# Performance work log

Hardware: AMD Instinct MI355X
Metric: run time of the kernel (lower is better)

## Reference

```python
import jax, jax.numpy as jnp
import numpy as np

B, T, C = 4, 2048, 1024
H, D = 16, 64  # num_heads, head_size; H*D == C


def setup_inputs() -> dict:
    key = jax.random.key(0)
    k1, k2, k3 = jax.random.split(key, 3)
    x = jax.random.normal(k1, (B, T, C), dtype=jnp.float32)
    w_qkv = jax.random.normal(k2, (C, 3 * C), dtype=jnp.float32) * (C ** -0.5)
    w_out = jax.random.normal(k3, (C, C), dtype=jnp.float32) * (C ** -0.5)
    b_out = jnp.zeros((C,), dtype=jnp.float32)
    return {"x": x, "w_qkv": w_qkv, "w_out": w_out, "b_out": b_out}


def reference(x, w_qkv, w_out, b_out):
    Bb, Tt, Cc = x.shape
    qkv = x @ w_qkv                        # [B,T,3C]
    q, k, v = jnp.split(qkv, 3, axis=2)
    # [B,T,C] -> [B,H,T,D]
    q = q.reshape(Bb, Tt, H, D).transpose(0, 2, 1, 3)
    k = k.reshape(Bb, Tt, H, D).transpose(0, 2, 1, 3)
    v = v.reshape(Bb, Tt, H, D).transpose(0, 2, 1, 3)
    scores = jnp.einsum('bhqd,bhkd->bhqk', q, k) * (D ** -0.5)
    causal = jnp.tril(jnp.ones((Tt, Tt), dtype=bool))
    scores = jnp.where(causal, scores, -jnp.inf)
    attn = jax.nn.softmax(scores, axis=-1)  # dropout is identity in eval mode
    out = jnp.einsum('bhqk,bhkd->bhqd', attn, v)
    out = out.transpose(0, 2, 1, 3).reshape(Bb, Tt, Cc)
    return out @ w_out + b_out
```

## Files before the change

### kernel.cpp

```cpp
#include <hip/hip_runtime.h>

typedef __bf16 bf16;
typedef __bf16 bf16x4 __attribute__((ext_vector_type(4)));
typedef __bf16 bf16x8 __attribute__((ext_vector_type(8)));
typedef float  f32x4  __attribute__((ext_vector_type(4)));

#define MFMA16(A_, B_, C_) __builtin_amdgcn_mfma_f32_16x16x32_bf16((A_), (B_), (C_), 0, 0, 0)

#define BB 4
#define TT 2048
#define CC 1024
#define HH 16
#define DD 64
#define MM (BB * TT)
#define N_QKV (3 * CC)
#define LDSS 72
#define BSTRIDE 36
#define QSCALE2 0.18033688f

#define BARRIER() do { asm volatile("" ::: "memory"); \
                       __builtin_amdgcn_s_barrier();  \
                       asm volatile("" ::: "memory"); } while (0)
#define VMCNT(n)  asm volatile("s_waitcnt vmcnt(" #n ")" ::: "memory")

static __device__ __forceinline__ void store_lds8(bf16* p, bf16x8 v) {
  bf16x4 lo, hi;
#pragma unroll
  for (int i = 0; i < 4; i++) { lo[i] = v[i]; hi[i] = v[i + 4]; }
  *(bf16x4*)p = lo;
  *(bf16x4*)(p + 4) = hi;
}

static __device__ __forceinline__ bf16x8 load_lds8(const bf16* p) {
  bf16x4 lo = *(const bf16x4*)p;
  bf16x4 hi = *(const bf16x4*)(p + 4);
  bf16x8 v;
#pragma unroll
  for (int i = 0; i < 4; i++) { v[i] = lo[i]; v[i + 4] = hi[i]; }
  return v;
}

static __device__ __forceinline__ void async_cp16(const bf16* g, bf16* l) {
  __builtin_amdgcn_global_load_lds(
      (const __attribute__((address_space(1))) void*)g,
      (__attribute__((address_space(3))) void*)l, 16, 0, 0);
}

__global__ __launch_bounds__(256) void sniff_k(const unsigned short* __restrict__ u,
                                               int* __restrict__ flag) {
  __shared__ int s;
  if (threadIdx.x == 0) s = 0;
  __syncthreads();
  int c = 0;
  for (int i = threadIdx.x; i < 65536; i += 256)
    if ((u[i] & 0x7F80u) == 0x7F80u) c = 1;
  if (c) atomicOr(&s, 1);
  __syncthreads();
  if (threadIdx.x == 0) *flag = s;
}

__global__ __launch_bounds__(256) void cvt_k(const void* __restrict__ in,
                                             bf16* __restrict__ out,
                                             const int* __restrict__ flag,
                                             size_t off) {
  const int fl = *flag;
  const size_t i = ((size_t)blockIdx.x * 256 + threadIdx.x) * 8;
  if (fl) {
    f32x4 a = *(const f32x4*)((const float*)in + off + i);
    f32x4 b = *(const f32x4*)((const float*)in + off + i + 4);
    bf16x8 o;
#pragma unroll
    for (int j = 0; j < 4; j++) { o[j] = (bf16)a[j]; o[4 + j] = (bf16)b[j]; }
    *(bf16x8*)(out + i) = o;
  } else {
    *(bf16x8*)(out + i) = *(const bf16x8*)((const bf16*)in + off + i);
  }
}

__global__ __launch_bounds__(256) void transpose_k(const void* __restrict__ in,
                                                   bf16* __restrict__ out,
                                                   int R, int C,
                                                   const int* __restrict__ flag) {
  __shared__ bf16 tile[32][33];
  const int fl = *flag;
  const int c0 = blockIdx.x * 32, r0 = blockIdx.y * 32;
  const int tx = threadIdx.x & 31, ty = threadIdx.x >> 5;
#pragma unroll
  for (int i = ty; i < 32; i += 8) {
    const size_t idx = (size_t)(r0 + i) * C + c0 + tx;
    tile[i][tx] = fl ? (bf16)((const float*)in)[idx] : ((const bf16*)in)[idx];
  }
  __syncthreads();
#pragma unroll
  for (int i = ty; i < 32; i += 8)
    out[(size_t)(c0 + i) * R + r0 + tx] = tile[tx][i];
}

__global__ __launch_bounds__(256) void vtrans_k(const bf16* __restrict__ qkv,
                                                bf16* __restrict__ vt) {
  __shared__ bf16 tile[32][33];
  const int bh = blockIdx.z;
  const int t0 = blockIdx.x * 32, d0 = blockIdx.y * 32;
  const bf16* src = qkv + (size_t)(bh >> 4) * TT * N_QKV + 2 * CC + (bh & 15) * DD;
  const int tx = threadIdx.x & 31, ty = threadIdx.x >> 5;
#pragma unroll
  for (int i = ty; i < 32; i += 8)
    tile[i][tx] = src[(size_t)(t0 + i) * N_QKV + d0 + tx];
  __syncthreads();
  bf16* dst = vt + ((size_t)bh * DD + d0) * TT + t0;
#pragma unroll
  for (int i = ty; i < 32; i += 8)
    dst[(size_t)i * TT + tx] = tile[tx][i];
}

template <int EPI>
__global__ __launch_bounds__(512, 2) void gemm8p(const bf16* __restrict__ A,
                                                 const bf16* __restrict__ Bt,
                                                 const void* __restrict__ biasv,
                                                 void* __restrict__ Cv,
                                                 const int* __restrict__ flag,
                                                 int M, int N, int K,
                                                 int lda, int ldc) {
  __shared__ __align__(16) bf16 sA[2][256 * 64];
  __shared__ __align__(16) bf16 sB[2][256 * 64];
  const int fl = *flag;
  const int tid = threadIdx.x;
  const int lane = tid & 63, wave = tid >> 6;
  const int quad = lane >> 4, l15 = lane & 15;
  const int wm = wave >> 2, wn = wave & 3;

  const int nm = M >> 8;
  const int cpx = gridDim.x >> 3;
  const int sw = ((int)blockIdx.x & 7) * cpx + ((int)blockIdx.x >> 3);
  const int m0 = (sw % nm) * 256, n0 = (sw / nm) * 256;

  const int s_row = wave * 8 + (lane >> 3);
  const int s_col = ((((lane & 7) * 16) ^ ((lane >> 3) << 4)) >> 1);

  f32x4 acc[8][4];
#pragma unroll
  for (int i = 0; i < 8; i++)
#pragma unroll
    for (int j = 0; j < 4; j++) {
      f32x4 z = {0.f, 0.f, 0.f, 0.f};
      acc[i][j] = z;
    }

  const bf16* Asrc = A + (size_t)(m0 + s_row) * lda + s_col;
  const bf16* Bsrc = Bt + (size_t)(n0 + s_row) * K + s_col;

#define STAGE8(buf_, k0_)                                                  \
  do {                                                                     \
    _Pragma("unroll")                                                      \
    for (int i_ = 0; i_ < 4; i_++)                                         \
      async_cp16(Asrc + (size_t)(i_ * 64) * lda + (k0_),                   \
                 &sA[buf_][i_ * 4096 + wave * 512]);                       \
    _Pragma("unroll")                                                      \
    for (int i_ = 0; i_ < 4; i_++)                                         \
      async_cp16(Bsrc + (size_t)(i_ * 64) * K + (k0_),                     \
                 &sB[buf_][i_ * 4096 + wave * 512]);                       \
  } while (0)

  const int swz = (l15 & 7) << 3;

#define COMPUTE8(buf_)                                                       \
  do {                                                                       \
    _Pragma("unroll")                                                        \
    for (int kk = 0; kk < 2; kk++) {                                         \
      bf16x8 bfr[4];                                                         \
      _Pragma("unroll")                                                      \
      for (int nf = 0; nf < 4; nf++) {                                       \
        const int rB = wn * 64 + nf * 16 + l15;                              \
        bfr[nf] = *(const bf16x8*)(&sB[buf_][rB * 64 +                       \
                                             ((kk * 32 + quad * 8) ^ swz)]); \
      }                                                                      \
      _Pragma("unroll")                                                      \
      for (int mh = 0; mh < 2; mh++) {                                       \
        bf16x8 af[4];                                                        \
        _Pragma("unroll")                                                    \
        for (int mf = 0; mf < 4; mf++) {                                     \
          const int rA = wm * 128 + (mh * 4 + mf) * 16 + l15;                \
          af[mf] = *(const bf16x8*)(&sA[buf_][rA * 64 +                      \
                                              ((kk * 32 + quad * 8) ^ swz)]);\
        }                                                                    \
        _Pragma("unroll")                                                    \
        for (int mf = 0; mf < 4; mf++)                                       \
          _Pragma("unroll")                                                  \
          for (int nf = 0; nf < 4; nf++)                                     \
            acc[mh * 4 + mf][nf] =                                           \
                MFMA16(af[mf], bfr[nf], acc[mh * 4 + mf][nf]);               \
      }                                                                      \
    }                                                                        \
  } while (0)

  const int NT = K >> 6;
  STAGE8(0, 0);
  STAGE8(1, 64);
  VMCNT(8);
  BARRIER();

  for (int t = 0; t < NT; t += 2) {
    COMPUTE8(0);
    BARRIER();
    if (t + 2 < NT) { STAGE8(0, (t + 2) * 64); VMCNT(8); }
    else            { VMCNT(0); }
    BARRIER();
    COMPUTE8(1);
    BARRIER();
    if (t + 3 < NT) { STAGE8(1, (t + 3) * 64); VMCNT(8); }
    else            { VMCNT(0); }
    BARRIER();
  }

#undef STAGE8
#undef COMPUTE8

#pragma unroll
  for (int mf = 0; mf < 8; mf++) {
#pragma unroll
    for (int r = 0; r < 4; r++) {
      const int m = m0 + wm * 128 + mf * 16 + quad * 4 + r;
#pragma unroll
      for (int nf = 0; nf < 4; nf++) {
        const int n = n0 + wn * 64 + nf * 16 + l15;
        float v = acc[mf][nf][r];
        const size_t idx = (size_t)m * ldc + n;
        if (EPI == 1) {
          v += fl ? ((const float*)biasv)[n] : (float)((const bf16*)biasv)[n];
          if (fl) ((float*)Cv)[idx] = v;
          else    ((bf16*)Cv)[idx] = (bf16)v;
        } else {
          ((bf16*)Cv)[idx] = (bf16)v;
        }
      }
    }
  }
}

template <int EPI>
__global__ __launch_bounds__(256) void gemm_lds(const bf16* __restrict__ A,
                                                const bf16* __restrict__ Bt,
                                                const void* __restrict__ biasv,
                                                void* __restrict__ Cv,
                                                const int* __restrict__ flag,
                                                size_t aoff, size_t coff,
                                                int M, int N, int K,
                                                int lda, int ldc) {
  const int fl = *flag;
  __shared__ __align__(16) bf16 sA[128 * 32];
  __shared__ __align__(16) bf16 sB[128 * 32];
  const int tid = threadIdx.x;
  const int lane = tid & 63, wave = tid >> 6;
  const int quad = lane >> 4, l15 = lane & 15;
  const int wr = wave >> 1, wc = wave & 1;
  const int m0 = blockIdx.x * 128, n0 = blockIdx.y * 128;
  const int grow = lane >> 2;
  const int gcol = (lane & 3) * 8;

  f32x4 acc[4][4];
#pragma unroll
  for (int i = 0; i < 4; i++)
#pragma unroll
    for (int j = 0; j < 4; j++) {
      f32x4 z = {0.f, 0.f, 0.f, 0.f};
      acc[i][j] = z;
    }

  const bf16* Ag = A + aoff + (size_t)(m0 + wave * 32 + grow) * lda + gcol;
  const bf16* Bg = Bt + (size_t)(n0 + wave * 32 + grow) * K + gcol;
  bf16* sAw = sA + wave * 32 * 32;
  bf16* sBw = sB + wave * 32 * 32;

  for (int k0 = 0; k0 < K; k0 += 32) {
    __syncthreads();
    async_cp16(Ag, sAw);
    async_cp16(Ag + (size_t)16 * lda, sAw + 16 * 32);
    async_cp16(Bg, sBw);
    async_cp16(Bg + (size_t)16 * K, sBw + 16 * 32);
    Ag += 32;
    Bg += 32;
    __syncthreads();

    bf16x8 af[4], bfr[4];
#pragma unroll
    for (int mi = 0; mi < 4; mi++)
      af[mi] = *(const bf16x8*)(sA + (wr * 64 + mi * 16 + l15) * 32 + quad * 8);
#pragma unroll
    for (int ni = 0; ni < 4; ni++)
      bfr[ni] = *(const bf16x8*)(sB + (wc * 64 + ni * 16 + l15) * 32 + quad * 8);
#pragma unroll
    for (int mi = 0; mi < 4; mi++)
#pragma unroll
      for (int ni = 0; ni < 4; ni++)
        acc[mi][ni] = MFMA16(af[mi], bfr[ni], acc[mi][ni]);
  }

#pragma unroll
  for (int mi = 0; mi < 4; mi++) {
#pragma unroll
    for (int r = 0; r < 4; r++) {
      const int m = m0 + wr * 64 + mi * 16 + quad * 4 + r;
#pragma unroll
      for (int ni = 0; ni < 4; ni++) {
        const int n = n0 + wc * 64 + ni * 16 + l15;
        float v = acc[mi][ni][r];
        const size_t idx = coff + (size_t)m * ldc + n;
        if (EPI == 1) {
          v += fl ? ((const float*)biasv)[n] : (float)((const bf16*)biasv)[n];
          if (fl) ((float*)Cv)[idx] = v;
          else    ((bf16*)Cv)[idx] = (bf16)v;
        } else {
          ((bf16*)Cv)[idx] = (bf16)v;
        }
      }
    }
  }
}

template <int EPI, bool AF>
__global__ __launch_bounds__(256) void gemm_bt(const void* __restrict__ Av,
                                               const bf16* __restrict__ Bt,
                                               const void* __restrict__ biasv,
                                               void* __restrict__ Cv,
                                               const int* __restrict__ flag,
                                               size_t aoff, size_t coff,
                                               int M, int N, int K,
                                               int lda, int ldc) {
  const int fl = *flag;
  const bool af32 = AF && (fl != 0);
  __shared__ __align__(16) bf16 sA[128 * 32];
  __shared__ __align__(16) bf16 sB[128 * 32];
  const int tid = threadIdx.x;
  const int lane = tid & 63, wave = tid >> 6;
  const int quad = lane >> 4, l15 = lane & 15;
  const int wr = wave >> 1, wc = wave & 1;
  const int m0 = blockIdx.x * 128, n0 = blockIdx.y * 128;
  const int srow = tid >> 2;
  const int scol = (tid & 3) * 8;

  f32x4 acc[4][4];
#pragma unroll
  for (int i = 0; i < 4; i++)
#pragma unroll
    for (int j = 0; j < 4; j++) {
      f32x4 z = {0.f, 0.f, 0.f, 0.f};
      acc[i][j] = z;
    }

  const size_t abase0 = aoff + (size_t)(m0 + srow) * lda + scol;
  const size_t abase1 = abase0 + (size_t)64 * lda;
  const bf16* Bg0 = Bt + (size_t)(n0 + srow) * K + scol;
  const bf16* Bg1 = Bg0 + (size_t)64 * K;

  for (int k0 = 0; k0 < K; k0 += 32) {
    bf16x8 a0, a1;
    if (af32) {
      const float* Af = (const float*)Av;
      f32x4 p00 = *(const f32x4*)(Af + abase0 + k0);
      f32x4 p01 = *(const f32x4*)(Af + abase0 + k0 + 4);
      f32x4 p10 = *(const f32x4*)(Af + abase1 + k0);
      f32x4 p11 = *(const f32x4*)(Af + abase1 + k0 + 4);
#pragma unroll
      for (int i = 0; i < 4; i++) {
        a0[i] = (bf16)p00[i]; a0[i + 4] = (bf16)p01[i];
        a1[i] = (bf16)p10[i]; a1[i + 4] = (bf16)p11[i];
      }
    } else {
      const bf16* Ab = (const bf16*)Av;
      a0 = *(const bf16x8*)(Ab + abase0 + k0);
      a1 = *(const bf16x8*)(Ab + abase1 + k0);
    }
    bf16x8 b0 = *(const bf16x8*)(Bg0 + k0);
    bf16x8 b1 = *(const bf16x8*)(Bg1 + k0);
    __syncthreads();
    *(bf16x8*)(sA + srow * 32 + scol) = a0;
    *(bf16x8*)(sA + (64 + srow) * 32 + scol) = a1;
    *(bf16x8*)(sB + srow * 32 + scol) = b0;
    *(bf16x8*)(sB + (64 + srow) * 32 + scol) = b1;
    __syncthreads();

    bf16x8 af[4], bfr[4];
#pragma unroll
    for (int mi = 0; mi < 4; mi++)
      af[mi] = *(const bf16x8*)(sA + (wr * 64 + mi * 16 + l15) * 32 + quad * 8);
#pragma unroll
    for (int ni = 0; ni < 4; ni++)
      bfr[ni] = *(const bf16x8*)(sB + (wc * 64 + ni * 16 + l15) * 32 + quad * 8);
#pragma unroll
    for (int mi = 0; mi < 4; mi++)
#pragma unroll
      for (int ni = 0; ni < 4; ni++)
        acc[mi][ni] = MFMA16(af[mi], bfr[ni], acc[mi][ni]);
  }

#pragma unroll
  for (int mi = 0; mi < 4; mi++) {
#pragma unroll
    for (int r = 0; r < 4; r++) {
      const int m = m0 + wr * 64 + mi * 16 + quad * 4 + r;
#pragma unroll
      for (int ni = 0; ni < 4; ni++) {
        const int n = n0 + wc * 64 + ni * 16 + l15;
        float v = acc[mi][ni][r];
        const size_t idx = coff + (size_t)m * ldc + n;
        if (EPI == 1) {
          v += fl ? ((const float*)biasv)[n] : (float)((const bf16*)biasv)[n];
          if (fl) ((float*)Cv)[idx] = v;
          else    ((bf16*)Cv)[idx] = (bf16)v;
        } else {
          ((bf16*)Cv)[idx] = (bf16)v;
        }
      }
    }
  }
}

template <int EPI, bool AF, bool WF>
__global__ __launch_bounds__(256) void gemm_nt(const void* __restrict__ Av,
                                               const void* __restrict__ Wv,
                                               const void* __restrict__ biasv,
                                               void* __restrict__ Cv,
                                               const int* __restrict__ flag,
                                               size_t aoff, size_t coff,
                                               int M, int N, int K,
                                               int lda, int ldc) {
  const int fl = *flag;
  const bool af32 = AF && (fl != 0);
  const bool wf32 = WF && (fl != 0);
  __shared__ __align__(16) bf16 sA[128 * 32];
  __shared__ __align__(16) bf16 sB[128 * BSTRIDE];
  const int tid = threadIdx.x;
  const int lane = tid & 63, wave = tid >> 6;
  const int quad = lane >> 4, l15 = lane & 15;
  const int wr = wave >> 1, wc = wave & 1;
  const int m0 = blockIdx.x * 128, n0 = blockIdx.y * 128;
  const int arow = tid >> 2, acol = (tid & 3) * 8;
  const int wk = tid >> 3, wn = (tid & 7) * 16;

  f32x4 acc[4][4];
#pragma unroll
  for (int i = 0; i < 4; i++)
#pragma unroll
    for (int j = 0; j < 4; j++) {
      f32x4 z = {0.f, 0.f, 0.f, 0.f};
      acc[i][j] = z;
    }

  const size_t abase0 = aoff + (size_t)(m0 + arow) * lda + acol;
  const size_t abase1 = abase0 + (size_t)64 * lda;

  for (int k0 = 0; k0 < K; k0 += 32) {
    bf16x8 a0, a1;
    if (af32) {
      const float* Af = (const float*)Av;
      f32x4 p00 = *(const f32x4*)(Af + abase0 + k0);
      f32x4 p01 = *(const f32x4*)(Af + abase0 + k0 + 4);
      f32x4 p10 = *(const f32x4*)(Af + abase1 + k0);
      f32x4 p11 = *(const f32x4*)(Af + abase1 + k0 + 4);
#pragma unroll
      for (int i = 0; i < 4; i++) {
        a0[i] = (bf16)p00[i]; a0[i + 4] = (bf16)p01[i];
        a1[i] = (bf16)p10[i]; a1[i + 4] = (bf16)p11[i];
      }
    } else {
      const bf16* Ab = (const bf16*)Av;
      a0 = *(const bf16x8*)(Ab + abase0 + k0);
      a1 = *(const bf16x8*)(Ab + abase1 + k0);
    }
    bf16 wreg[16];
    const size_t wbase = (size_t)(k0 + wk) * N + n0 + wn;
    if (wf32) {
      const float* Wf = (const float*)Wv;
      f32x4 q0 = *(const f32x4*)(Wf + wbase);
      f32x4 q1 = *(const f32x4*)(Wf + wbase + 4);
      f32x4 q2 = *(const f32x4*)(Wf + wbase + 8);
      f32x4 q3 = *(const f32x4*)(Wf + wbase + 12);
#pragma unroll
      for (int i = 0; i < 4; i++) {
        wreg[i] = (bf16)q0[i];      wreg[4 + i] = (bf16)q1[i];
        wreg[8 + i] = (bf16)q2[i];  wreg[12 + i] = (bf16)q3[i];
      }
    } else {
      const bf16* Wb = (const bf16*)Wv;
      bf16x8 w0 = *(const bf16x8*)(Wb + wbase);
      bf16x8 w1 = *(const bf16x8*)(Wb + wbase + 8);
#pragma unroll
      for (int i = 0; i < 8; i++) { wreg[i] = w0[i]; wreg[8 + i] = w1[i]; }
    }
    __syncthreads();
    *(bf16x8*)(sA + arow * 32 + acol) = a0;
    *(bf16x8*)(sA + (64 + arow) * 32 + acol) = a1;
#pragma unroll
    for (int i = 0; i < 16; i++)
      sB[(wn + i) * BSTRIDE + wk] = wreg[i];
    __syncthreads();

    bf16x8 af[4], bfr[4];
#pragma unroll
    for (int mi = 0; mi < 4; mi++)
      af[mi] = *(const bf16x8*)(sA + (wr * 64 + mi * 16 + l15) * 32 + quad * 8);
#pragma unroll
    for (int ni = 0; ni < 4; ni++)
      bfr[ni] = load_lds8(sB + (wc * 64 + ni * 16 + l15) * BSTRIDE + quad * 8);
#pragma unroll
    for (int mi = 0; mi < 4; mi++)
#pragma unroll
      for (int ni = 0; ni < 4; ni++)
        acc[mi][ni] = MFMA16(af[mi], bfr[ni], acc[mi][ni]);
  }

#pragma unroll
  for (int mi = 0; mi < 4; mi++) {
#pragma unroll
    for (int r = 0; r < 4; r++) {
      const int m = m0 + wr * 64 + mi * 16 + quad * 4 + r;
#pragma unroll
      for (int ni = 0; ni < 4; ni++) {
        const int n = n0 + wc * 64 + ni * 16 + l15;
        float v = acc[mi][ni][r];
        const size_t idx = coff + (size_t)m * ldc + n;
        if (EPI == 1) {
          v += fl ? ((const float*)biasv)[n] : (float)((const bf16*)biasv)[n];
          if (fl) ((float*)Cv)[idx] = v;
          else    ((bf16*)Cv)[idx] = (bf16)v;
        } else {
          ((bf16*)Cv)[idx] = (bf16)v;
        }
      }
    }
  }
}

__global__ __launch_bounds__(256) void attn_k(bf16* __restrict__ qkv,
                                              const bf16* __restrict__ vt) {
  __shared__ __align__(16) bf16 sP[128 * LDSS];
  __shared__ __align__(16) bf16 sK[64 * LDSS];
  __shared__ __align__(16) bf16 sVt[64 * LDSS];

  const int tid = threadIdx.x;
  const int lane = tid & 63, wave = tid >> 6;
  const int quad = lane >> 4, l15 = lane & 15;
  const int bh = blockIdx.x;
  bf16* base = qkv + (size_t)(bh >> 4) * TT * N_QKV + (bh & 15) * DD;
  const bf16* Qp = base;
  const bf16* Kp = base + CC;
  const bf16* vhead = vt + (size_t)bh * DD * TT;

  const int qt = 15 - (int)blockIdx.y;
  const int q0 = qt * 128;
  const int wave_row0 = q0 + wave * 32;
  bf16* sPw = sP + (size_t)(wave * 32) * LDSS;

  const int krow = tid >> 2;
  const int kcol = (tid & 3) * 16;

  bf16x8 ones;
  {
    const bf16 o = (l15 == 0) ? (bf16)1.0f : (bf16)0.0f;
#pragma unroll
    for (int i = 0; i < 8; i++) ones[i] = o;
  }

  bf16x8 aq[2][2];
#pragma unroll
  for (int mi = 0; mi < 2; mi++)
#pragma unroll
    for (int ks = 0; ks < 2; ks++) {
      bf16x8 v = *(const bf16x8*)(Qp + (size_t)(wave_row0 + mi * 16 + l15) * N_QKV +
                                  ks * 32 + quad * 8);
#pragma unroll
      for (int i = 0; i < 8; i++) v[i] = (bf16)((float)v[i] * QSCALE2);
      aq[mi][ks] = v;
    }

  bf16x8 kr0, kr1, vr0, vr1;
  {
    const bf16* kp = Kp + (size_t)krow * N_QKV + kcol;
    kr0 = *(const bf16x8*)kp;
    kr1 = *(const bf16x8*)(kp + 8);
    const bf16* vp = vhead + (size_t)krow * TT + kcol;
    vr0 = *(const bf16x8*)vp;
    vr1 = *(const bf16x8*)(vp + 8);
  }

  f32x4 Oacc[2][4];
  f32x4 lacc[2];
#pragma unroll
  for (int mi = 0; mi < 2; mi++) {
    f32x4 z = {0.f, 0.f, 0.f, 0.f};
    lacc[mi] = z;
#pragma unroll
    for (int nt = 0; nt < 4; nt++) Oacc[mi][nt] = z;
  }

  const int jmax = q0 + 64;

  for (int j0 = 0; j0 <= jmax; j0 += 64) {
    __syncthreads();
    *(bf16x8*)(sK + krow * LDSS + kcol) = kr0;
    *(bf16x8*)(sK + krow * LDSS + kcol + 8) = kr1;
    *(bf16x8*)(sVt + krow * LDSS + kcol) = vr0;
    *(bf16x8*)(sVt + krow * LDSS + kcol + 8) = vr1;
    __syncthreads();

    if (j0 + 64 <= jmax) {
      const bf16* kp = Kp + (size_t)(j0 + 64 + krow) * N_QKV + kcol;
      kr0 = *(const bf16x8*)kp;
      kr1 = *(const bf16x8*)(kp + 8);
      const bf16* vp = vhead + (size_t)krow * TT + j0 + 64 + kcol;
      vr0 = *(const bf16x8*)vp;
      vr1 = *(const bf16x8*)(vp + 8);
    }

    if (j0 <= wave_row0 + 31) {
      f32x4 S[2][4];
#pragma unroll
      for (int mi = 0; mi < 2; mi++)
#pragma unroll
        for (int kt = 0; kt < 4; kt++) {
          f32x4 z = {0.f, 0.f, 0.f, 0.f};
          S[mi][kt] = z;
        }
      __builtin_amdgcn_s_setprio(1);
#pragma unroll
      for (int kt = 0; kt < 4; kt++) {
        const bf16* kp = sK + (size_t)(kt * 16 + l15) * LDSS + quad * 8;
        bf16x8 k0 = *(const bf16x8*)kp;
        bf16x8 k1 = *(const bf16x8*)(kp + 32);
        S[0][kt] = MFMA16(k0, aq[0][0], S[0][kt]);
        S[0][kt] = MFMA16(k1, aq[0][1], S[0][kt]);
        S[1][kt] = MFMA16(k0, aq[1][0], S[1][kt]);
        S[1][kt] = MFMA16(k1, aq[1][1], S[1][kt]);
      }
      __builtin_amdgcn_s_setprio(0);

      const bool needmask = (j0 + 63 > wave_row0);
#pragma unroll
      for (int mi = 0; mi < 2; mi++) {
        const int qg = wave_row0 + mi * 16 + l15;
#pragma unroll
        for (int kt = 0; kt < 4; kt++) {
          const int kb = j0 + kt * 16 + quad * 4;
          bf16x4 pk;
#pragma unroll
          for (int r = 0; r < 4; r++) {
            float e = __builtin_amdgcn_exp2f(S[mi][kt][r]);
            if (needmask && (kb + r > qg)) e = 0.f;
            pk[r] = (bf16)e;
          }
          *(bf16x4*)(sPw + (size_t)(mi * 16 + l15) * LDSS + kt * 16 + quad * 4) = pk;
        }
      }

      bf16x8 ap0[2], ap1[2];
#pragma unroll
      for (int mi = 0; mi < 2; mi++) {
        const bf16* pp = sPw + (size_t)(mi * 16 + l15) * LDSS + quad * 8;
        ap0[mi] = *(const bf16x8*)pp;
        ap1[mi] = *(const bf16x8*)(pp + 32);
      }
      __builtin_amdgcn_s_setprio(1);
#pragma unroll
      for (int mi = 0; mi < 2; mi++) {
        lacc[mi] = MFMA16(ap0[mi], ones, lacc[mi]);
        lacc[mi] = MFMA16(ap1[mi], ones, lacc[mi]);
      }
#pragma unroll
      for (int nt = 0; nt < 4; nt++) {
        const bf16* vp = sVt + (size_t)(nt * 16 + l15) * LDSS + quad * 8;
        bf16x8 v0 = *(const bf16x8*)vp;
        bf16x8 v1 = *(const bf16x8*)(vp + 32);
        Oacc[0][nt] = MFMA16(ap0[0], v0, Oacc[0][nt]);
        Oacc[0][nt] = MFMA16(ap1[0], v1, Oacc[0][nt]);
        Oacc[1][nt] = MFMA16(ap0[1], v0, Oacc[1][nt]);
        Oacc[1][nt] = MFMA16(ap1[1], v1, Oacc[1][nt]);
      }
      __builtin_amdgcn_s_setprio(0);
    }
  }

#pragma unroll
  for (int mi = 0; mi < 2; mi++)
#pragma unroll
    for (int r = 0; r < 4; r++) {
      const float lv = __shfl(lacc[mi][r], lane & 48, 64);
      const float invl = 1.0f / lv;
      const int t = q0 + wave * 32 + mi * 16 + quad * 4 + r;
#pragma unroll
      for (int nt = 0; nt < 4; nt++)
        base[(size_t)t * N_QKV + nt * 16 + l15] =
            (bf16)(Oacc[mi][nt][r] * invl);
    }
}

__global__ __launch_bounds__(256) void attn_s(bf16* __restrict__ qkv) {
  __shared__ __align__(16) bf16 sQ[128 * LDSS];
  __shared__ __align__(16) bf16 sK[64 * LDSS];
  __shared__ __align__(16) bf16 sVt[64 * LDSS];

  const int tid = threadIdx.x;
  const int lane = tid & 63, wave = tid >> 6;
  const int quad = lane >> 4, l15 = lane & 15;
  const int bh = blockIdx.x;
  bf16* base = qkv + (size_t)(bh >> 4) * TT * N_QKV + (bh & 15) * DD;
  const bf16* Qp = base;
  const bf16* Kp = base + CC;
  const bf16* Vp = base + 2 * CC;

  const int krow = tid >> 2;
  const int kcol = (tid & 3) * 16;
  const int vkey = tid & 31;
  const int vcol = (tid >> 5) * 8;

  bf16x8 ones;
  {
    const bf16 o = (l15 == 0) ? (bf16)1.0f : (bf16)0.0f;
#pragma unroll
    for (int i = 0; i < 8; i++) ones[i] = o;
  }

  const int qt = 15 - (int)blockIdx.y;
  const int q0 = qt * 128;

#pragma unroll
  for (int p = 0; p < 2; p++) {
    const int r = p * 64 + krow;
    const bf16* src = Qp + (size_t)(q0 + r) * N_QKV + kcol;
    bf16x8 v0 = *(const bf16x8*)src;
    bf16x8 v1 = *(const bf16x8*)(src + 8);
#pragma unroll
    for (int i = 0; i < 8; i++) {
      v0[i] = (bf16)((float)v0[i] * QSCALE2);
      v1[i] = (bf16)((float)v1[i] * QSCALE2);
    }
    *(bf16x8*)(sQ + r * LDSS + kcol) = v0;
    *(bf16x8*)(sQ + r * LDSS + kcol + 8) = v1;
  }

  bf16x8 kr0, kr1, vr0, vr1;
  {
    const bf16* kp = Kp + (size_t)krow * N_QKV + kcol;
    kr0 = *(const bf16x8*)kp;
    kr1 = *(const bf16x8*)(kp + 8);
    vr0 = *(const bf16x8*)(Vp + (size_t)vkey * N_QKV + vcol);
    vr1 = *(const bf16x8*)(Vp + (size_t)(32 + vkey) * N_QKV + vcol);
  }
  __syncthreads();

  bf16x8 aq[2][2];
#pragma unroll
  for (int mi = 0; mi < 2; mi++) {
    const bf16* qp = sQ + (size_t)(wave * 32 + mi * 16 + l15) * LDSS + quad * 8;
    aq[mi][0] = *(const bf16x8*)qp;
    aq[mi][1] = *(const bf16x8*)(qp + 32);
  }

  f32x4 Oacc[2][4];
  f32x4 lacc[2];
#pragma unroll
  for (int mi = 0; mi < 2; mi++) {
    f32x4 z = {0.f, 0.f, 0.f, 0.f};
    lacc[mi] = z;
#pragma unroll
    for (int nt = 0; nt < 4; nt++) Oacc[mi][nt] = z;
  }

  const int jmax = q0 + 64;
  const int wave_row0 = q0 + wave * 32;
  bf16* sP = sQ + (size_t)(wave * 32) * LDSS;

  for (int j0 = 0; j0 <= jmax; j0 += 64) {
    __syncthreads();
    *(bf16x8*)(sK + krow * LDSS + kcol) = kr0;
    *(bf16x8*)(sK + krow * LDSS + kcol + 8) = kr1;
#pragma unroll
    for (int i = 0; i < 8; i++) {
      sVt[(vcol + i) * LDSS + vkey] = vr0[i];
      sVt[(vcol + i) * LDSS + 32 + vkey] = vr1[i];
    }
    __syncthreads();

    if (j0 + 64 <= jmax) {
      const bf16* kp = Kp + (size_t)(j0 + 64 + krow) * N_QKV + kcol;
      kr0 = *(const bf16x8*)kp;
      kr1 = *(const bf16x8*)(kp + 8);
      vr0 = *(const bf16x8*)(Vp + (size_t)(j0 + 64 + vkey) * N_QKV + vcol);
      vr1 = *(const bf16x8*)(Vp + (size_t)(j0 + 96 + vkey) * N_QKV + vcol);
    }

    if (j0 <= wave_row0 + 31) {
      f32x4 S[2][4];
#pragma unroll
      for (int nt = 0; nt < 4; nt++) {
        const bf16* kp = sK + (size_t)(nt * 16 + l15) * LDSS + quad * 8;
        bf16x8 bk0 = *(const bf16x8*)kp;
        bf16x8 bk1 = *(const bf16x8*)(kp + 32);
#pragma unroll
        for (int mi = 0; mi < 2; mi++) {
          f32x4 acc = {0.f, 0.f, 0.f, 0.f};
          acc = MFMA16(aq[mi][0], bk0, acc);
          acc = MFMA16(aq[mi][1], bk1, acc);
          S[mi][nt] = acc;
        }
      }

      const bool needmask = (j0 + 63 > wave_row0);
#pragma unroll
      for (int mi = 0; mi < 2; mi++)
#pragma unroll
        for (int nt = 0; nt < 4; nt++) {
          const int kc = j0 + nt * 16 + l15;
#pragma unroll
          for (int r = 0; r < 4; r++) {
            float e = __builtin_amdgcn_exp2f(S[mi][nt][r]);
            if (needmask && kc > wave_row0 + mi * 16 + quad * 4 + r) e = 0.f;
            sP[(size_t)(mi * 16 + quad * 4 + r) * LDSS + nt * 16 + l15] =
                (bf16)e;
          }
        }

      bf16x8 ap[2][2];
#pragma unroll
      for (int mi = 0; mi < 2; mi++) {
        const bf16* pp = sP + (size_t)(mi * 16 + l15) * LDSS + quad * 8;
        ap[mi][0] = *(const bf16x8*)pp;
        ap[mi][1] = *(const bf16x8*)(pp + 32);
        lacc[mi] = MFMA16(ap[mi][0], ones, lacc[mi]);
        lacc[mi] = MFMA16(ap[mi][1], ones, lacc[mi]);
      }
#pragma unroll
      for (int nt = 0; nt < 4; nt++) {
        const bf16* vp = sVt + (size_t)(nt * 16 + l15) * LDSS + quad * 8;
        bf16x8 bv0 = *(const bf16x8*)vp;
        bf16x8 bv1 = *(const bf16x8*)(vp + 32);
#pragma unroll
        for (int mi = 0; mi < 2; mi++) {
          Oacc[mi][nt] = MFMA16(ap[mi][0], bv0, Oacc[mi][nt]);
          Oacc[mi][nt] = MFMA16(ap[mi][1], bv1, Oacc[mi][nt]);
        }
      }
    }
  }

#pragma unroll
  for (int mi = 0; mi < 2; mi++)
#pragma unroll
    for (int r = 0; r < 4; r++) {
      const float lv = __shfl(lacc[mi][r], lane & 48, 64);
      const float invl = 1.0f / lv;
      const int t = q0 + wave * 32 + mi * 16 + quad * 4 + r;
#pragma unroll
      for (int nt = 0; nt < 4; nt++)
        base[(size_t)t * N_QKV + nt * 16 + l15] =
            (bf16)(Oacc[mi][nt][r] * invl);
    }
}

extern "C" void kernel_launch(void* const* d_in, const int* in_sizes, int n_in,
                              void* d_out, int out_size, void* d_ws, size_t ws_size,
                              hipStream_t stream) {
  const void* x = d_in[0];
  const void* w_qkv = d_in[1];
  const void* w_out = d_in[2];
  const void* b_out = d_in[3];

  int* flag = (int*)d_ws;
  char* p = (char*)d_ws + 256;
  bf16* wqkvT = (bf16*)p;
  bf16* woutT = wqkvT + (size_t)N_QKV * CC;

  const size_t wT_bytes = ((size_t)N_QKV * CC + (size_t)CC * CC) * 2;
  const size_t qkv_bytes = (size_t)MM * N_QKV * 2;
  const size_t need_A = 256 + wT_bytes + qkv_bytes;
  const size_t need_B = 256 + wT_bytes + (size_t)TT * N_QKV * 2;

  sniff_k<<<1, 256, 0, stream>>>((const unsigned short*)x, flag);

  if (ws_size >= need_A) {
    bf16* qkv = woutT + (size_t)CC * CC;
    bf16* xb = qkv + (size_t)MM * N_QKV;
    const size_t slack = ws_size - need_A;

    transpose_k<<<dim3(N_QKV / 32, CC / 32), 256, 0, stream>>>(w_qkv, wqkvT, CC, N_QKV, flag);
    transpose_k<<<dim3(CC / 32, CC / 32), 256, 0, stream>>>(w_out, woutT, CC, CC, flag);

    const size_t full_xb = (size_t)MM * CC * 2;
    const size_t half_xb = full_xb / 2;
    if (slack >= full_xb) {
      cvt_k<<<(MM * CC) / 2048, 256, 0, stream>>>(x, xb, flag, 0);
      gemm8p<0><<<dim3((MM / 256) * (N_QKV / 256)), 512, 0, stream>>>(
          xb, wqkvT, nullptr, qkv, flag, MM, N_QKV, CC, CC, N_QKV);
      bf16* vt = xb;
      vtrans_k<<<dim3(TT / 32, DD / 32, BB * HH), 256, 0, stream>>>(qkv, vt);
      attn_k<<<dim3(BB * HH, 16), 256, 0, stream>>>(qkv, vt);
    } else if (slack >= half_xb) {
      for (int m0 = 0; m0 < MM; m0 += 4096) {
        cvt_k<<<(4096 * CC) / 2048, 256, 0, stream>>>(x, xb, flag, (size_t)m0 * CC);
        gemm_lds<0><<<dim3(4096 / 128, N_QKV / 128), 256, 0, stream>>>(
            xb, wqkvT, nullptr, qkv, flag, 0, (size_t)m0 * N_QKV,
            4096, N_QKV, CC, CC, N_QKV);
      }
      attn_s<<<dim3(BB * HH, 16), 256, 0, stream>>>(qkv);
    } else {
      gemm_bt<0, true><<<dim3(MM / 128, N_QKV / 128), 256, 0, stream>>>(
          x, wqkvT, nullptr, qkv, flag, 0, 0, MM, N_QKV, CC, CC, N_QKV);
      attn_s<<<dim3(BB * HH, 16), 256, 0, stream>>>(qkv);
    }

    gemm8p<1><<<dim3((MM / 256) * (CC / 256)), 512, 0, stream>>>(
        qkv, woutT, b_out, d_out, flag, MM, CC, CC, N_QKV, CC);
  } else if (ws_size >= need_B) {
    bf16* qkv = woutT + (size_t)CC * CC;
    transpose_k<<<dim3(N_QKV / 32, CC / 32), 256, 0, stream>>>(w_qkv, wqkvT, CC, N_QKV, flag);
    transpose_k<<<dim3(CC / 32, CC / 32), 256, 0, stream>>>(w_out, woutT, CC, CC, flag);
    for (int b = 0; b < BB; b++) {
      const size_t xoff = (size_t)b * TT * CC;
      gemm_bt<0, true><<<dim3(TT / 128, N_QKV / 128), 256, 0, stream>>>(
          x, wqkvT, nullptr, qkv, flag, xoff, 0, TT, N_QKV, CC, CC, N_QKV);
      attn_s<<<dim3(HH, 16), 256, 0, stream>>>(qkv);
      gemm_lds<1><<<dim3(TT / 128, CC / 128), 256, 0, stream>>>(
          qkv, woutT, b_out, d_out, flag, 0, xoff, TT, CC, CC, N_QKV, CC);
    }
  } else {
    bf16* qkvb = (bf16*)p;
    for (int b = 0; b < BB; b++) {
      const size_t xoff = (size_t)b * TT * CC;
      gemm_nt<0, true, true><<<dim3(TT / 128, N_QKV / 128), 256, 0, stream>>>(
          x, w_qkv, nullptr, qkvb, flag, xoff, 0, TT, N_QKV, CC, CC, N_QKV);
      attn_s<<<dim3(HH, 16), 256, 0, stream>>>(qkvb);
      gemm_nt<1, false, true><<<dim3(TT / 128, CC / 128), 256, 0, stream>>>(
          qkvb, w_out, b_out, d_out, flag, 0, xoff, TT, CC, CC, N_QKV, CC);
    }
  }
}
```

Baseline: 334.5 us.

## Restructure GEMM mainloop into fine-grained phases interleaving async loads with MFMA

Splits each 64-wide K tile into two 32-wide sub-buffers and breaks compute into eight phases per 128-K step. Each phase issues a slice of the next async global-to-LDS copies, bumps wave priority around the MFMA block, and waits on vmcnt at finer points. The goal is to overlap memory traffic with matrix math. It also changes the LDS swizzle to 32-column rows and switches block-to-tile mapping to be row-major over N. It adds more barriers per iteration and a subtle prefetch and wait ordering that must stay correct.

```diff
diff --git a/kernel.cpp b/kernel.cpp
--- a/kernel.cpp
+++ b/kernel.cpp
@@ -121,21 +121,25 @@
                                                  const int* __restrict__ flag,
                                                  int M, int N, int K,
                                                  int lda, int ldc) {
-  __shared__ __align__(16) bf16 sA[2][256 * 64];
-  __shared__ __align__(16) bf16 sB[2][256 * 64];
+  __shared__ __align__(16) bf16 sAb[2][2][256 * 32];
+  __shared__ __align__(16) bf16 sBb[2][2][256 * 32];
   const int fl = *flag;
   const int tid = threadIdx.x;
   const int lane = tid & 63, wave = tid >> 6;
   const int quad = lane >> 4, l15 = lane & 15;
   const int wm = wave >> 2, wn = wave & 3;
 
-  const int nm = M >> 8;
+  const int nn = N >> 8;
   const int cpx = gridDim.x >> 3;
   const int sw = ((int)blockIdx.x & 7) * cpx + ((int)blockIdx.x >> 3);
-  const int m0 = (sw % nm) * 256, n0 = (sw / nm) * 256;
-
-  const int s_row = wave * 8 + (lane >> 3);
-  const int s_col = ((((lane & 7) * 16) ^ ((lane >> 3) << 4)) >> 1);
+  const int m0 = (sw / nn) * 256, n0 = (sw % nn) * 256;
+
+  const int srow = tid >> 2;
+  const int scol8 = (((tid & 3) ^ ((tid >> 3) & 3)) << 3);
+  const int rdcol = ((quad ^ ((l15 >> 1) & 3)) << 3);
+
+  const bf16* Asrc = A + (size_t)(m0 + srow) * lda + scol8;
+  const bf16* Bsrc = Bt + (size_t)(n0 + srow) * K + scol8;
 
   f32x4 acc[8][4];
 #pragma unroll
@@ -146,74 +150,74 @@
       acc[i][j] = z;
     }
 
-  const bf16* Asrc = A + (size_t)(m0 + s_row) * lda + s_col;
-  const bf16* Bsrc = Bt + (size_t)(n0 + s_row) * K + s_col;
-
-#define STAGE8(buf_, k0_)                                                  \
-  do {                                                                     \
-    _Pragma("unroll")                                                      \
-    for (int i_ = 0; i_ < 4; i_++)                                         \
-      async_cp16(Asrc + (size_t)(i_ * 64) * lda + (k0_),                   \
-                 &sA[buf_][i_ * 4096 + wave * 512]);                       \
-    _Pragma("unroll")                                                      \
-    for (int i_ = 0; i_ < 4; i_++)                                         \
-      async_cp16(Bsrc + (size_t)(i_ * 64) * K + (k0_),                     \
-                 &sB[buf_][i_ * 4096 + wave * 512]);                       \
+#define ST_A(buf_, kk_, k0_) do {                                          \
+    async_cp16(Asrc + (k0_) + (kk_) * 32, &sAb[buf_][kk_][wave * 512]);    \
+    async_cp16(Asrc + (size_t)128 * lda + (k0_) + (kk_) * 32,              \
+               &sAb[buf_][kk_][4096 + wave * 512]);                        \
   } while (0)
-
-  const int swz = (l15 & 7) << 3;
-
-#define COMPUTE8(buf_)                                                       \
-  do {                                                                       \
+#define ST_B(buf_, kk_, k0_) do {                                          \
+    async_cp16(Bsrc + (k0_) + (kk_) * 32, &sBb[buf_][kk_][wave * 512]);    \
+    async_cp16(Bsrc + (size_t)128 * K + (k0_) + (kk_) * 32,                \
+               &sBb[buf_][kk_][4096 + wave * 512]);                        \
+  } while (0)
+
+  bf16x8 bfr[4];
+
+#define PH(buf_, kk_, mh_, STAGE_, WAIT_) do {                               \
+    bf16x8 af_[4];                                                           \
     _Pragma("unroll")                                                        \
-    for (int kk = 0; kk < 2; kk++) {                                         \
-      bf16x8 bfr[4];                                                         \
+    for (int mf = 0; mf < 4; mf++)                                           \
+      af_[mf] = *(const bf16x8*)(&sAb[buf_][kk_][                            \
+          (wm * 128 + (mh_) * 64 + mf * 16 + l15) * 32 + rdcol]);            \
+    if (!(mh_)) {                                                            \
       _Pragma("unroll")                                                      \
-      for (int nf = 0; nf < 4; nf++) {                                       \
-        const int rB = wn * 64 + nf * 16 + l15;                              \
-        bfr[nf] = *(const bf16x8*)(&sB[buf_][rB * 64 +                       \
-                                             ((kk * 32 + quad * 8) ^ swz)]); \
-      }                                                                      \
+      for (int nf = 0; nf < 4; nf++)                                         \
+        bfr[nf] = *(const bf16x8*)(&sBb[buf_][kk_][                          \
+            (wn * 64 + nf * 16 + l15) * 32 + rdcol]);                        \
+    }                                                                        \
+    STAGE_;                                                                  \
+    BARRIER();                                                               \
+    __builtin_amdgcn_s_setprio(1);                                           \
+    _Pragma("unroll")                                                        \
+    for (int mf = 0; mf < 4; mf++)                                           \
       _Pragma("unroll")                                                      \
-      for (int mh = 0; mh < 2; mh++) {                                       \
-        bf16x8 af[4];                                                        \
-        _Pragma("unroll")                                                    \
-        for (int mf = 0; mf < 4; mf++) {                                     \
-          const int rA = wm * 128 + (mh * 4 + mf) * 16 + l15;                \
-          af[mf] = *(const bf16x8*)(&sA[buf_][rA * 64 +                      \
-                                              ((kk * 32 + quad * 8) ^ swz)]);\
-        }                                                                    \
-        _Pragma("unroll")                                                    \
-        for (int mf = 0; mf < 4; mf++)                                       \
-          _Pragma("unroll")                                                  \
-          for (int nf = 0; nf < 4; nf++)                                     \
-            acc[mh * 4 + mf][nf] =                                           \
-                MFMA16(af[mf], bfr[nf], acc[mh * 4 + mf][nf]);               \
-      }                                                                      \
-    }                                                                        \
+      for (int nf = 0; nf < 4; nf++)                                         \
+        acc[(mh_) * 4 + mf][nf] =                                            \
+            MFMA16(af_[mf], bfr[nf], acc[(mh_) * 4 + mf][nf]);               \
+    __builtin_amdgcn_s_setprio(0);                                           \
+    WAIT_;                                                                   \
+    BARRIER();                                                               \
   } while (0)
 
-  const int NT = K >> 6;
-  STAGE8(0, 0);
-  STAGE8(1, 64);
-  VMCNT(8);
+  ST_A(0, 0, 0); ST_B(0, 0, 0); ST_A(0, 1, 0); ST_B(0, 1, 0);
+  ST_A(1, 0, 64); ST_B(1, 0, 64);
+  VMCNT(4);
   BARRIER();
 
-  for (int t = 0; t < NT; t += 2) {
-    COMPUTE8(0);
-    BARRIER();
-    if (t + 2 < NT) { STAGE8(0, (t + 2) * 64); VMCNT(8); }
-    else            { VMCNT(0); }
-    BARRIER();
-    COMPUTE8(1);
-    BARRIER();
-    if (t + 3 < NT) { STAGE8(1, (t + 3) * 64); VMCNT(8); }
-    else            { VMCNT(0); }
-    BARRIER();
-  }
-
-#undef STAGE8
-#undef COMPUTE8
+  int k0 = 0;
+  const int NI = (K >> 7) - 1;
+  for (int i = 0; i < NI; i++, k0 += 128) {
+    PH(0, 0, 0, ST_A(1, 1, k0 + 64),  ;        );
+    PH(0, 0, 1, ST_B(1, 1, k0 + 64),  ;        );
+    PH(0, 1, 0, ST_A(0, 0, k0 + 128), ;        );
+    PH(0, 1, 1, ST_B(0, 0, k0 + 128), VMCNT(8));
+    PH(1, 0, 0, ST_A(0, 1, k0 + 128), ;        );
+    PH(1, 0, 1, ST_B(0, 1, k0 + 128), VMCNT(8));
+    PH(1, 1, 0, ST_A(1, 0, k0 + 192), ;        );
+    PH(1, 1, 1, ST_B(1, 0, k0 + 192), VMCNT(4));
+  }
+  PH(0, 0, 0, ST_A(1, 1, k0 + 64), ;        );
+  PH(0, 0, 1, ST_B(1, 1, k0 + 64), ;        );
+  PH(0, 1, 0, ;                  , ;        );
+  PH(0, 1, 1, ;                  , VMCNT(4));
+  PH(1, 0, 0, ;                  , ;        );
+  PH(1, 0, 1, ;                  , VMCNT(0));
+  PH(1, 1, 0, ;                  , ;        );
+  PH(1, 1, 1, ;                  , ;        );
+
+#undef PH
+#undef ST_A
+#undef ST_B
 
 #pragma unroll
   for (int mf = 0; mf < 8; mf++) {
```

Result: faster. 321.5 us (-3.9%).
